# Kernel tuning notes

Measured on AMD Instinct MI355X. Metric: run time of the kernel, lower is better.

Reference implementation:

```python
import jax, jax.numpy as jnp
import numpy as np

N_HEAD = 16
N_EMBD = 1024


def setup_inputs() -> dict:
    key = jax.random.key(0)
    k1, k2 = jax.random.split(key)
    x = jax.random.normal(k1, (2, 2048, N_EMBD), dtype=jnp.float32)
    # nn.Linear(n_embd, 3*n_embd, bias=False); store as [in, out] for x @ w
    w_qkv = jax.random.normal(k2, (N_EMBD, 3 * N_EMBD), dtype=jnp.float32) * (N_EMBD ** -0.5)
    return {"x": x, "w_qkv": w_qkv}


def reference(x, w_qkv):
    B, T, C = x.shape
    H = N_HEAD
    D = C // H  # head dim
    qkv = x @ w_qkv  # [B, T, 3C]
    q, k, v = jnp.split(qkv, 3, axis=2)
    # [B, T, H, D] -> [B, H, T, D]
    q = q.reshape(B, T, H, D).transpose(0, 2, 1, 3)
    k = k.reshape(B, T, H, D).transpose(0, 2, 1, 3)
    v = v.reshape(B, T, H, D).transpose(0, 2, 1, 3)
    att = jnp.einsum('bhtd,bhsd->bhts', q, k) / np.sqrt(D).astype(np.float32)
    causal = jnp.tril(jnp.ones((T, T), dtype=bool))  # [T, T]
    att = jnp.where(causal, att, -jnp.inf)
    att = jax.nn.softmax(att, axis=-1)
    out = jnp.einsum('bhts,bhsd->bhtd', att, v)  # [B, H, T, D]
    return out.transpose(0, 2, 1, 3).reshape(B, T, C)
```

## Files before the change

### kernel.cpp

```cpp
#include <hip/hip_runtime.h>
#include <hip/hip_bf16.h>

#define BATCH 2
#define SEQ   2048
#define EMBD  1024
#define NHEAD 16
#define HDIM  64
#define N3    3072
#define MTOT  4096
#define KDIM  1024

typedef __attribute__((ext_vector_type(8))) short  short8;
typedef __attribute__((ext_vector_type(4))) short  s16x4;
typedef __attribute__((ext_vector_type(4))) float  f32x4;

__device__ __forceinline__ short f2bfs(float f) {
    return __builtin_bit_cast(short, __float2bfloat16(f));
}

__global__ __launch_bounds__(256) void cast_x_kernel(const float* __restrict__ x,
                                                     short* __restrict__ xb, int n4) {
    int i = blockIdx.x * 256 + threadIdx.x;
    if (i >= n4) return;
    float4 f = reinterpret_cast<const float4*>(x)[i];
    s16x4 o;
    o[0] = f2bfs(f.x); o[1] = f2bfs(f.y);
    o[2] = f2bfs(f.z); o[3] = f2bfs(f.w);
    reinterpret_cast<s16x4*>(xb)[i] = o;
}

__global__ __launch_bounds__(256) void cast_wt_kernel(const float* __restrict__ w,
                                                      short* __restrict__ wt) {
    __shared__ float tile[32][33];
    int n0 = blockIdx.x * 32;
    int k0 = blockIdx.y * 32;
    int tx = threadIdx.x & 31;
    int ty = threadIdx.x >> 5;
#pragma unroll
    for (int i = 0; i < 4; ++i)
        tile[ty + i * 8][tx] = w[(size_t)(k0 + ty + i * 8) * N3 + n0 + tx];
    __syncthreads();
#pragma unroll
    for (int i = 0; i < 4; ++i)
        wt[(size_t)(n0 + ty + i * 8) * KDIM + k0 + tx] = f2bfs(tile[tx][ty + i * 8]);
}

__device__ __forceinline__ void stage_tile(const short* gbase, short* lbase, int tid) {
#pragma unroll
    for (int c = 0; c < 2; ++c) {
        int row = c * 64 + (tid >> 2);
        int chunk = (tid & 3) ^ ((row >> 1) & 3);
        const short* gp = gbase + (size_t)row * KDIM + chunk * 8;
        short* lp = lbase + c * 2048 + tid * 8;
        __builtin_amdgcn_global_load_lds((const __attribute__((address_space(1))) void*)gp,
                                         (__attribute__((address_space(3))) void*)lp,
                                         16, 0, 0);
    }
}

__global__ __launch_bounds__(256) void qkv_gemm_kernel(const short* __restrict__ xb,
                                                       const short* __restrict__ wt,
                                                       short* __restrict__ qb,
                                                       short* __restrict__ kbuf,
                                                       short* __restrict__ vt) {
    __shared__ short lA[2][128 * 32];
    __shared__ short lB[2][128 * 32];

    const int tid  = threadIdx.x;
    const int lane = tid & 63;
    const int wid  = tid >> 6;
    const int wm = wid >> 1, wn = wid & 1;
    const int lid = blockIdx.x;
    const int swz = (lid & 7) * 96 + (lid >> 3);
    const int m0 = (swz / 24) * 128;
    const int n0 = (swz % 24) * 128;

    f32x4 acc[4][4];
#pragma unroll
    for (int i = 0; i < 4; ++i)
#pragma unroll
        for (int j = 0; j < 4; ++j) acc[i][j] = (f32x4){0.f, 0.f, 0.f, 0.f};

    const short* gA = xb + (size_t)m0 * KDIM;
    const short* gB = wt + (size_t)n0 * KDIM;

    stage_tile(gA, lA[0], tid);
    stage_tile(gB, lB[0], tid);
    asm volatile("s_waitcnt vmcnt(0)" ::: "memory");
    __syncthreads();

    int cur = 0;
    const int arow = (lane & 15) * 32 + (((lane >> 4) ^ ((lane >> 1) & 3)) * 8);
#pragma unroll 1
    for (int kt = 0; kt < KDIM / 32; ++kt) {
        if (kt + 1 < KDIM / 32) {
            stage_tile(gA + (kt + 1) * 32, lA[cur ^ 1], tid);
            stage_tile(gB + (kt + 1) * 32, lB[cur ^ 1], tid);
        }
        short8 a[4], b[4];
#pragma unroll
        for (int im = 0; im < 4; ++im)
            a[im] = *(const short8*)&lA[cur][(wm * 64 + im * 16) * 32 + arow];
#pragma unroll
        for (int in = 0; in < 4; ++in)
            b[in] = *(const short8*)&lB[cur][(wn * 64 + in * 16) * 32 + arow];
#pragma unroll
        for (int im = 0; im < 4; ++im)
#pragma unroll
            for (int in = 0; in < 4; ++in)
                acc[im][in] = __builtin_amdgcn_mfma_f32_16x16x32_bf16(a[im], b[in], acc[im][in], 0, 0, 0);
        asm volatile("s_waitcnt vmcnt(0)" ::: "memory");
        __syncthreads();
        cur ^= 1;
    }

#pragma unroll
    for (int im = 0; im < 4; ++im) {
        int t0m = m0 + wm * 64 + im * 16 + (lane >> 4) * 4;
        int b = t0m >> 11;
        int t0 = t0m & 2047;
#pragma unroll
        for (int in = 0; in < 4; ++in) {
            int col = n0 + wn * 64 + in * 16 + (lane & 15);
            int which = col >> 10;
            int h = (col >> 6) & 15;
            int d = col & 63;
            if (which == 2) {
                s16x4 pk;
#pragma unroll
                for (int r = 0; r < 4; ++r) pk[r] = f2bfs(acc[im][in][r]);
                *(s16x4*)&vt[((size_t)(b * NHEAD + h) * HDIM + d) * SEQ + t0] = pk;
            } else {
                short* dst = (which == 0) ? qb : kbuf;
#pragma unroll
                for (int r = 0; r < 4; ++r)
                    dst[((size_t)(b * NHEAD + h) * SEQ + t0 + r) * HDIM + d] = f2bfs(acc[im][in][r]);
            }
        }
    }
}

#define KVB 64

__device__ __forceinline__ int swzf(int r) { return (r & 3) ^ (((r >> 2) & 3) << 1); }

__device__ __forceinline__ void stage_kv(const short* kh, const short* vh, int kb,
                                         short* lk, short* lv, int tid) {
#pragma unroll
    for (int c = 0; c < 2; ++c) {
        int row = c * 32 + (tid >> 3);
        int sch = (tid & 7) ^ swzf(row);
        const short* gk = kh + (size_t)(kb + row) * HDIM + sch * 8;
        short* lpk = lk + c * 2048 + tid * 8;
        __builtin_amdgcn_global_load_lds((const __attribute__((address_space(1))) void*)gk,
                                         (__attribute__((address_space(3))) void*)lpk, 16, 0, 0);
        const short* gv = vh + (size_t)row * SEQ + kb + sch * 8;
        short* lpv = lv + c * 2048 + tid * 8;
        __builtin_amdgcn_global_load_lds((const __attribute__((address_space(1))) void*)gv,
                                         (__attribute__((address_space(3))) void*)lpv, 16, 0, 0);
    }
}

__global__ __launch_bounds__(256) void attn_kernel(const short* __restrict__ q,
                                                   const short* __restrict__ kk,
                                                   const short* __restrict__ vtg,
                                                   float* __restrict__ out) {
    const int tid  = threadIdx.x;
    const int lane = tid & 63;
    const int wid  = tid >> 6;
    const int lid  = blockIdx.x;
    const int xcd  = lid & 7;
    const int rest = lid >> 3;
    const int batch = rest >> 5;
    const int slot  = rest & 31;
    const int u     = slot >> 2;
    const int hrank = slot & 3;
    const int qt = (batch == 0) ? 31 - u : (batch == 1) ? 16 + u
                 : (batch == 2) ? 15 - u : u;
    const int bh = hrank * 8 + xcd;
    const int rbase = lane & 15;
    const int hi    = lane >> 4;

    const short* qh = q   + (size_t)bh * SEQ * HDIM;
    const short* kh = kk  + (size_t)bh * SEQ * HDIM;
    const short* vh = vtg + (size_t)bh * HDIM * SEQ;

    __shared__ short lK[2][KVB * 64];
    __shared__ short lV[2][KVB * 64];

    const float L2E = 1.4426950408889634f;
    const float C1  = 0.125f * 1.4426950408889634f;
    short8 vone;
#pragma unroll
    for (int j = 0; j < 8; ++j) vone[j] = (short)0x3F80;

    const int b = bh >> 4, h = bh & 15;

    const int qbase = qt * 64 + wid * 16;
    const int qrow  = qbase + rbase;

    short8 aQ[2];
#pragma unroll
    for (int c = 0; c < 2; ++c)
        aQ[c] = *(const short8*)&qh[(size_t)qrow * HDIM + c * 32 + hi * 8];

    f32x4 o[4];
#pragma unroll
    for (int i = 0; i < 4; ++i) o[i] = (f32x4){0.f, 0.f, 0.f, 0.f};
    float mrun = -INFINITY;
    float lrun = 0.f;

    const int ktiles = qt + 1;
    stage_kv(kh, vh, 0, lK[0], lV[0], tid);
    int cur = 0;
#pragma unroll 1
    for (int t = 0; t < ktiles; ++t) {
        const int kb = t * KVB;
        if (t + 1 < ktiles) {
            stage_kv(kh, vh, kb + KVB, lK[cur ^ 1], lV[cur ^ 1], tid);
            asm volatile("s_waitcnt vmcnt(4) lgkmcnt(0)" ::: "memory");
        } else {
            asm volatile("s_waitcnt vmcnt(0) lgkmcnt(0)" ::: "memory");
        }
        __builtin_amdgcn_s_barrier();
        __builtin_amdgcn_sched_barrier(0);

        if (kb < qbase + 16) {
            const short* lk = lK[cur];
            const short* lv = lV[cur];
            f32x4 s[4];
            __builtin_amdgcn_s_setprio(1);
#pragma unroll
            for (int nb = 0; nb < 4; ++nb) {
                int kidx = (nb & 1) * 32 + (rbase >> 2) * 8 + (nb >> 1) * 4 + (rbase & 3);
                f32x4 a = (f32x4){0.f, 0.f, 0.f, 0.f};
#pragma unroll
                for (int c = 0; c < 2; ++c) {
                    int slot2 = (c * 4 + hi) ^ swzf(kidx);
                    short8 bK = *(const short8*)&lk[kidx * 64 + slot2 * 8];
                    a = __builtin_amdgcn_mfma_f32_16x16x32_bf16(bK, aQ[c], a, 0, 0, 0);
                }
                s[nb] = a;
            }
            __builtin_amdgcn_s_setprio(0);
            if (kb + KVB - 1 > qbase) {
#pragma unroll
                for (int nb = 0; nb < 4; ++nb) {
                    int keyb = kb + (nb & 1) * 32 + hi * 8 + (nb >> 1) * 4;
#pragma unroll
                    for (int r = 0; r < 4; ++r)
                        if (keyb + r > qrow) s[nb][r] = -1e30f;
                }
            }
            float pm = fmaxf(fmaxf(fmaxf(s[0][0], s[0][1]), fmaxf(s[0][2], s[0][3])),
                             fmaxf(fmaxf(s[1][0], s[1][1]), fmaxf(s[1][2], s[1][3])));
            float pm2 = fmaxf(fmaxf(fmaxf(s[2][0], s[2][1]), fmaxf(s[2][2], s[2][3])),
                              fmaxf(fmaxf(s[3][0], s[3][1]), fmaxf(s[3][2], s[3][3])));
            pm = fmaxf(pm, pm2);
            pm = fmaxf(pm, __shfl_xor(pm, 16));
            pm = fmaxf(pm, __shfl_xor(pm, 32));
            pm *= 0.125f;
            if (__any(pm > mrun + 8.0f)) {
                float mnew = fmaxf(mrun, pm);
                float sf = exp2f((mrun - mnew) * L2E);
                mrun = mnew;
                lrun *= sf;
#pragma unroll
                for (int dt = 0; dt < 4; ++dt)
#pragma unroll
                    for (int r = 0; r < 4; ++r) o[dt][r] *= sf;
            }
            float mterm = mrun * L2E;
            short8 bp[2];
#pragma unroll
            for (int c = 0; c < 2; ++c)
#pragma unroll
                for (int j = 0; j < 8; ++j) {
                    float p = exp2f(fmaf(s[c + (j >> 2) * 2][j & 3], C1, -mterm));
                    bp[c][j] = f2bfs(p);
                }
            f32x4 osum = (f32x4){0.f, 0.f, 0.f, 0.f};
            __builtin_amdgcn_s_setprio(1);
#pragma unroll
            for (int dt = 0; dt < 4; ++dt) {
                int d = dt * 16 + rbase;
#pragma unroll
                for (int c = 0; c < 2; ++c) {
                    int slot2 = (c * 4 + hi) ^ swzf(d);
                    short8 bV = *(const short8*)&lv[d * 64 + slot2 * 8];
                    o[dt] = __builtin_amdgcn_mfma_f32_16x16x32_bf16(bV, bp[c], o[dt], 0, 0, 0);
                }
            }
#pragma unroll
            for (int c = 0; c < 2; ++c)
                osum = __builtin_amdgcn_mfma_f32_16x16x32_bf16(vone, bp[c], osum, 0, 0, 0);
            __builtin_amdgcn_s_setprio(0);
            lrun += osum[0];
        }
        __builtin_amdgcn_sched_barrier(0);
        __builtin_amdgcn_s_barrier();
        cur ^= 1;
    }

    float inv = 1.0f / lrun;
#pragma unroll
    for (int dt = 0; dt < 4; ++dt) {
        f32x4 ov;
#pragma unroll
        for (int r = 0; r < 4; ++r) ov[r] = o[dt][r] * inv;
        *(f32x4*)&out[((size_t)(b * SEQ + qrow) * NHEAD + h) * HDIM + dt * 16 + hi * 4] = ov;
    }
}

extern "C" void kernel_launch(void* const* d_in, const int* in_sizes, int n_in,
                              void* d_out, int out_size, void* d_ws, size_t ws_size,
                              hipStream_t stream) {
    const float* x = (const float*)d_in[0];
    const float* w = (const float*)d_in[1];
    float* out = (float*)d_out;

    char* ws = (char*)d_ws;
    short* xb   = (short*)(ws);
    short* wt   = (short*)(ws + (size_t)8  * 1024 * 1024);
    short* qb   = (short*)(ws + (size_t)14 * 1024 * 1024);
    short* kbuf = (short*)(ws + (size_t)22 * 1024 * 1024);
    short* vt   = (short*)(ws + (size_t)30 * 1024 * 1024);

    cast_x_kernel<<<dim3(MTOT * KDIM / 4 / 256), dim3(256), 0, stream>>>(x, xb, MTOT * KDIM / 4);
    cast_wt_kernel<<<dim3(N3 / 32, KDIM / 32), dim3(256), 0, stream>>>(w, wt);
    qkv_gemm_kernel<<<dim3(768), dim3(256), 0, stream>>>(xb, wt, qb, kbuf, vt);
    attn_kernel<<<dim3(1024), dim3(256), 0, stream>>>(qb, kbuf, vt, out);
}
```

Baseline: 96.13 us.

## Add per-XCD atomic work queue for causal attention tiles, fold scale into Q

```diff
diff --git a/kernel.cpp b/kernel.cpp
--- a/kernel.cpp
+++ b/kernel.cpp
@@ -132,9 +132,10 @@
                 *(s16x4*)&vt[((size_t)(b * NHEAD + h) * HDIM + d) * SEQ + t0] = pk;
             } else {
                 short* dst = (which == 0) ? qb : kbuf;
+                float sc = (which == 0) ? 0.125f : 1.0f;
 #pragma unroll
                 for (int r = 0; r < 4; ++r)
-                    dst[((size_t)(b * NHEAD + h) * SEQ + t0 + r) * HDIM + d] = f2bfs(acc[im][in][r]);
+                    dst[((size_t)(b * NHEAD + h) * SEQ + t0 + r) * HDIM + d] = f2bfs(acc[im][in][r] * sc);
             }
         }
     }
@@ -164,20 +165,21 @@
 __global__ __launch_bounds__(256) void attn_kernel(const short* __restrict__ q,
                                                    const short* __restrict__ kk,
                                                    const short* __restrict__ vtg,
+                                                   unsigned int* __restrict__ queue,
                                                    float* __restrict__ out) {
     const int tid  = threadIdx.x;
     const int lane = tid & 63;
     const int wid  = tid >> 6;
-    const int lid  = blockIdx.x;
-    const int xcd  = lid & 7;
-    const int rest = lid >> 3;
-    const int batch = rest >> 5;
-    const int slot  = rest & 31;
-    const int u     = slot >> 2;
-    const int hrank = slot & 3;
-    const int qt = (batch == 0) ? 31 - u : (batch == 1) ? 16 + u
-                 : (batch == 2) ? 15 - u : u;
-    const int bh = hrank * 8 + xcd;
+    const int xcd  = blockIdx.x & 7;
+
+    __shared__ unsigned int sjob;
+    if (tid == 0) sjob = atomicAdd(&queue[xcd << 4], 1u);
+    __syncthreads();
+    const int j     = (int)sjob;
+    const int qt    = 31 - (j >> 2);
+    const int hrank = j & 3;
+    const int bh    = hrank * 8 + xcd;
+
     const int rbase = lane & 15;
     const int hi    = lane >> 4;
 
@@ -189,10 +191,9 @@
     __shared__ short lV[2][KVB * 64];
 
     const float L2E = 1.4426950408889634f;
-    const float C1  = 0.125f * 1.4426950408889634f;
     short8 vone;
 #pragma unroll
-    for (int j = 0; j < 8; ++j) vone[j] = (short)0x3F80;
+    for (int jj = 0; jj < 8; ++jj) vone[jj] = (short)0x3F80;
 
     const int b = bh >> 4, h = bh & 15;
 
@@ -218,9 +219,9 @@
         const int kb = t * KVB;
         if (t + 1 < ktiles) {
             stage_kv(kh, vh, kb + KVB, lK[cur ^ 1], lV[cur ^ 1], tid);
-            asm volatile("s_waitcnt vmcnt(4) lgkmcnt(0)" ::: "memory");
+            asm volatile("s_waitcnt vmcnt(4)" ::: "memory");
         } else {
-            asm volatile("s_waitcnt vmcnt(0) lgkmcnt(0)" ::: "memory");
+            asm volatile("s_waitcnt vmcnt(0)" ::: "memory");
         }
         __builtin_amdgcn_s_barrier();
         __builtin_amdgcn_sched_barrier(0);
@@ -259,7 +260,6 @@
             pm = fmaxf(pm, pm2);
             pm = fmaxf(pm, __shfl_xor(pm, 16));
             pm = fmaxf(pm, __shfl_xor(pm, 32));
-            pm *= 0.125f;
             if (__any(pm > mrun + 8.0f)) {
                 float mnew = fmaxf(mrun, pm);
                 float sf = exp2f((mrun - mnew) * L2E);
@@ -275,9 +275,9 @@
 #pragma unroll
             for (int c = 0; c < 2; ++c)
 #pragma unroll
-                for (int j = 0; j < 8; ++j) {
-                    float p = exp2f(fmaf(s[c + (j >> 2) * 2][j & 3], C1, -mterm));
-                    bp[c][j] = f2bfs(p);
+                for (int jj = 0; jj < 8; ++jj) {
+                    float p = exp2f(fmaf(s[c + (jj >> 2) * 2][jj & 3], L2E, -mterm));
+                    bp[c][jj] = f2bfs(p);
                 }
             f32x4 osum = (f32x4){0.f, 0.f, 0.f, 0.f};
             __builtin_amdgcn_s_setprio(1);
@@ -320,14 +320,16 @@
     float* out = (float*)d_out;
 
     char* ws = (char*)d_ws;
-    short* xb   = (short*)(ws);
-    short* wt   = (short*)(ws + (size_t)8  * 1024 * 1024);
-    short* qb   = (short*)(ws + (size_t)14 * 1024 * 1024);
-    short* kbuf = (short*)(ws + (size_t)22 * 1024 * 1024);
-    short* vt   = (short*)(ws + (size_t)30 * 1024 * 1024);
-
+    unsigned int* queue = (unsigned int*)ws;
+    short* xb   = (short*)(ws + (size_t)1  * 1024 * 1024);
+    short* wt   = (short*)(ws + (size_t)9  * 1024 * 1024);
+    short* qb   = (short*)(ws + (size_t)15 * 1024 * 1024);
+    short* kbuf = (short*)(ws + (size_t)23 * 1024 * 1024);
+    short* vt   = (short*)(ws + (size_t)31 * 1024 * 1024);
+
+    hipMemsetAsync(queue, 0, 512, stream);
     cast_x_kernel<<<dim3(MTOT * KDIM / 4 / 256), dim3(256), 0, stream>>>(x, xb, MTOT * KDIM / 4);
     cast_wt_kernel<<<dim3(N3 / 32, KDIM / 32), dim3(256), 0, stream>>>(w, wt);
     qkv_gemm_kernel<<<dim3(768), dim3(256), 0, stream>>>(xb, wt, qb, kbuf, vt);
-    attn_kernel<<<dim3(1024), dim3(256), 0, stream>>>(qb, kbuf, vt, out);
-}
+    attn_kernel<<<dim3(1024), dim3(256), 0, stream>>>(qb, kbuf, vt, queue, out);
+}
```

Result: slower. 122.1 us (+27.0%).
